# Performance work log

Measured on AMD Instinct MI355X. Metric: run time of the kernel, lower is better.

The kernel has to match this reference:

```python
import jax, jax.numpy as jnp
import numpy as np

N, E, IN, H, C = 20000, 320000, 512, 4, 64
HC = H * C
EPS_BN = 1e-5


def setup_inputs() -> dict:
    key = jax.random.key(0)
    ks = jax.random.split(key, 12)
    p = lambda k, shape, s=0.05: jax.random.normal(k, shape, dtype=jnp.float32) * s
    z = lambda n: jnp.zeros((n,), jnp.float32)
    o = lambda n: jnp.ones((n,), jnp.float32)
    return {
        "x": jax.random.normal(ks[0], (N, IN), dtype=jnp.float32),
        "edge_index": jax.random.randint(ks[1], (2, E), 0, N),
        "Wl0": p(ks[2], (IN, HC)), "Wr0": p(ks[3], (IN, HC)),
        "att0": p(ks[4], (H, C)), "b0": z(HC),
        "g0": o(HC), "be0": z(HC), "m0": z(HC), "v0": o(HC),
        "Wl1": p(ks[5], (HC, HC)), "Wr1": p(ks[6], (HC, HC)),
        "att1": p(ks[7], (H, C)), "b1": z(HC),
        "g1": o(HC), "be1": z(HC), "m1": z(HC), "v1": o(HC),
        "Wl2": p(ks[8], (HC, 2)), "Wr2": p(ks[9], (HC, 2)),
        "att2": p(ks[10], (1, 2)), "b2": z(2),
    }


def gatv2_conv(x, Wl, Wr, att, b, ei, concat):
    # GATv2: e_ij = att . LeakyReLU(Wl x_j + Wr x_i); softmax over in-edges of i
    n = x.shape[0]
    h, c = att.shape
    xl = (x @ Wl).reshape(n, h, c)  # source/message transform
    xr = (x @ Wr).reshape(n, h, c)  # target transform
    src, dst = ei[0], ei[1]
    m = xl[src] + xr[dst]                                   # [E,H,C] edge gather
    e = jnp.sum(jax.nn.leaky_relu(m, 0.2) * att, axis=-1)   # [E,H]
    emax = jax.ops.segment_max(e, dst, num_segments=n)      # segment softmax
    emax = jnp.where(jnp.isfinite(emax), emax, 0.0)
    ex = jnp.exp(e - emax[dst])
    denom = jax.ops.segment_sum(ex, dst, num_segments=n)
    alpha = ex / (denom[dst] + 1e-16)                       # [E,H]
    out = jax.ops.segment_sum(alpha[:, :, None] * xl[src], dst, num_segments=n)
    out = out.reshape(n, h * c) if concat else out.mean(axis=1)
    return out + b


def bn_eval(x, g, be, m, v):
    return (x - m) * (g * jax.lax.rsqrt(v + EPS_BN)) + be


def reference(x, edge_index, Wl0, Wr0, att0, b0, g0, be0, m0, v0,
              Wl1, Wr1, att1, b1, g1, be1, m1, v1, Wl2, Wr2, att2, b2):
    loops = jnp.arange(N)
    ei = jnp.concatenate([edge_index, jnp.stack([loops, loops])], axis=1)
    h = gatv2_conv(x, Wl0, Wr0, att0, b0, ei, True)
    h = jax.nn.elu(bn_eval(h, g0, be0, m0, v0))
    h = gatv2_conv(h, Wl1, Wr1, att1, b1, ei, True)
    h = jax.nn.elu(bn_eval(h, g1, be1, m1, v1))
    out = gatv2_conv(h, Wl2, Wr2, att2, b2, ei, False)
    return jax.nn.log_softmax(out, axis=1)
```

## Files before the change

kernel.cpp:

```cpp
#include <hip/hip_runtime.h>
#include <math.h>

#define NN 20000
#define MP 20096
#define EE 320000
#define ET (EE + NN)
#define HC 256
#define EPS_BN 1e-5f

typedef __bf16 bf16x8 __attribute__((ext_vector_type(8)));
typedef float f32x4 __attribute__((ext_vector_type(4)));

__device__ __forceinline__ float4 ld4(const float* p) { return *reinterpret_cast<const float4*>(p); }
__device__ __forceinline__ float lrelu(float x) { return fmaxf(x, 0.f) + 0.2f * fminf(x, 0.f); }

__device__ __forceinline__ unsigned short f2b(float f) {
  unsigned int u = __float_as_uint(f);
  u = (u + 0x7fffu + ((u >> 16) & 1u)) >> 16;
  return (unsigned short)u;
}
__device__ __forceinline__ float b2f(unsigned short u) {
  return __uint_as_float(((unsigned int)u) << 16);
}

__device__ __forceinline__ void gld_lds16(const void* g, void* l) {
  __builtin_amdgcn_global_load_lds(
      (const __attribute__((address_space(1))) unsigned int*)g,
      (__attribute__((address_space(3))) unsigned int*)(unsigned int)(unsigned long long)l,
      16, 0, 0);
}

#define CXB 5000
#define HB  ((ET + 255) / 256)
#define W0B 1024
#define W1B 512

__device__ __forceinline__ void conv_w_body(int idx, int K, const float* Wl, const float* Wr,
                                            unsigned short* Wf) {
  int n = idx / K, k = idx - n * K;
  float v = (n < 256) ? Wl[(size_t)k * 256 + n] : Wr[(size_t)k * 256 + (n - 256)];
  Wf[idx] = f2b(v);
}

__global__ __launch_bounds__(256) void prep_kernel(const float* __restrict__ x,
                                                   unsigned short* __restrict__ xb,
                                                   const int* __restrict__ ei,
                                                   int* __restrict__ counts,
                                                   const float* __restrict__ Wl0,
                                                   const float* __restrict__ Wr0,
                                                   unsigned short* __restrict__ Wf0,
                                                   const float* __restrict__ Wl1,
                                                   const float* __restrict__ Wr1,
                                                   unsigned short* __restrict__ Wf1) {
  const int b = blockIdx.x;
  if (b < CXB) {
    int i = (b * 256 + threadIdx.x) * 8;
    float4 v0 = ld4(&x[i]);
    float4 v1 = ld4(&x[i + 4]);
    ushort4 o0, o1;
    o0.x = f2b(v0.x); o0.y = f2b(v0.y); o0.z = f2b(v0.z); o0.w = f2b(v0.w);
    o1.x = f2b(v1.x); o1.y = f2b(v1.y); o1.z = f2b(v1.z); o1.w = f2b(v1.w);
    *reinterpret_cast<ushort4*>(&xb[i]) = o0;
    *reinterpret_cast<ushort4*>(&xb[i + 4]) = o1;
  } else if (b < CXB + HB) {
    int e = (b - CXB) * 256 + threadIdx.x;
    if (e < ET) {
      int d = (e < EE) ? ei[EE + e] : (e - EE);
      atomicAdd(&counts[d], 1);
    }
  } else if (b < CXB + HB + W0B) {
    conv_w_body((b - CXB - HB) * 256 + threadIdx.x, 512, Wl0, Wr0, Wf0);
  } else {
    conv_w_body((b - CXB - HB - W0B) * 256 + threadIdx.x, 256, Wl1, Wr1, Wf1);
  }
}

__global__ __launch_bounds__(512, 6) void gemm_mfma(const unsigned short* __restrict__ A,
                                                    const unsigned short* __restrict__ Bt,
                                                    unsigned short* __restrict__ xlb,
                                                    float* __restrict__ xrf,
                                                    int M, int K) {
  __shared__ unsigned short As[3][128 * 32];
  __shared__ unsigned short Bs[3][128 * 32];
  const int tid = threadIdx.x;
  const int wave = tid >> 6;
  const int lane = tid & 63;
  const int am = lane & 15;
  const int aq = lane >> 4;
  const int wr = (wave >> 2) * 64;
  const int wc = (wave & 3) * 32;

  const int nwg = gridDim.x;
  const int orig = blockIdx.x;
  const int q = nwg >> 3, r = nwg & 7;
  const int xcd = orig & 7, ii = orig >> 3;
  const int wgid = (xcd < r ? xcd * (q + 1) : r * (q + 1) + (xcd - r) * q) + ii;
  const int row0 = (wgid >> 2) * 128;
  const int col0 = (wgid & 3) * 128;

  const int r_ = tid >> 2;
  const int ks = (tid & 3) * 8;
  const size_t aoff = (size_t)(row0 + r_) * K + ks;
  const size_t boff = (size_t)(col0 + r_) * K + ks;

  const int nk = K >> 5;

#define STAGE(tt, bb)                                                    \
  do {                                                                   \
    gld_lds16(A + aoff + (size_t)(tt) * 32, &As[bb][wave * 512]);        \
    gld_lds16(Bt + boff + (size_t)(tt) * 32, &Bs[bb][wave * 512]);       \
  } while (0)

  f32x4 acc[4][2] = {};

  STAGE(0, 0);
  STAGE(1, 1);

  int cur = 0;
  int sb = 2;
  for (int t = 0; t < nk; ++t) {
    if (t + 1 < nk) {
      asm volatile("s_waitcnt vmcnt(2)" ::: "memory");
    } else {
      asm volatile("s_waitcnt vmcnt(0)" ::: "memory");
    }
    __builtin_amdgcn_s_barrier();
    __builtin_amdgcn_sched_barrier(0);

    if (t + 2 < nk) STAGE(t + 2, sb);

    bf16x8 af[4], bfr[2];
#pragma unroll
    for (int i = 0; i < 4; ++i)
      af[i] = *reinterpret_cast<const bf16x8*>(&As[cur][(wr + i * 16 + am) * 32 + aq * 8]);
#pragma unroll
    for (int j = 0; j < 2; ++j)
      bfr[j] = *reinterpret_cast<const bf16x8*>(&Bs[cur][(wc + j * 16 + am) * 32 + aq * 8]);
#pragma unroll
    for (int i = 0; i < 4; ++i)
#pragma unroll
      for (int j = 0; j < 2; ++j)
        acc[i][j] = __builtin_amdgcn_mfma_f32_16x16x32_bf16(af[i], bfr[j], acc[i][j], 0, 0, 0);

    cur = (cur == 2) ? 0 : cur + 1;
    sb = (sb == 2) ? 0 : sb + 1;
  }
#undef STAGE

#pragma unroll
  for (int i = 0; i < 4; ++i) {
#pragma unroll
    for (int j = 0; j < 2; ++j) {
      int gcol = col0 + wc + j * 16 + am;
#pragma unroll
      for (int rr = 0; rr < 4; ++rr) {
        int grow = row0 + wr + i * 16 + aq * 4 + rr;
        if (grow < M) {
          float v = acc[i][j][rr];
          if (gcol < 256) xlb[(size_t)grow * 256 + gcol] = f2b(v);
          else            xrf[(size_t)grow * 256 + (gcol - 256)] = v;
        }
      }
    }
  }
}

__global__ __launch_bounds__(1024) void scan_kernel(int* __restrict__ cursor,
                                                    int* __restrict__ offsets) {
  __shared__ int wsum[16];
  const int tid = threadIdx.x;
  const int lane = tid & 63, wv = tid >> 6;
  const int base = tid * 20;
  int vals[20];
  int s = 0;
  if (tid < 1000) {
#pragma unroll
    for (int j = 0; j < 20; ++j) { vals[j] = cursor[base + j]; s += vals[j]; }
  }
  int ssum = s;
#pragma unroll
  for (int off = 1; off < 64; off <<= 1) {
    int t = __shfl_up(ssum, off);
    if (lane >= off) ssum += t;
  }
  if (lane == 63) wsum[wv] = ssum;
  __syncthreads();
  if (wv == 0) {
    int w = (lane < 16) ? wsum[lane] : 0;
#pragma unroll
    for (int off = 1; off < 16; off <<= 1) {
      int t = __shfl_up(w, off);
      if (lane >= off) w += t;
    }
    if (lane < 16) wsum[lane] = w;
  }
  __syncthreads();
  int excl = ssum - s + (wv > 0 ? wsum[wv - 1] : 0);
  if (tid < 1000) {
    int run = excl;
#pragma unroll
    for (int j = 0; j < 20; ++j) { offsets[base + j] = run; cursor[base + j] = run; run += vals[j]; }
  }
  if (tid == 1023) offsets[NN] = wsum[15];
}

__global__ __launch_bounds__(256) void scatter_kernel(const int* __restrict__ ei,
                                                      int* __restrict__ cursor,
                                                      int* __restrict__ srcs) {
  int e = blockIdx.x * blockDim.x + threadIdx.x;
  if (e >= ET) return;
  int s, d;
  if (e < EE) { s = ei[e]; d = ei[EE + e]; } else { s = d = e - EE; }
  int pos = atomicAdd(&cursor[d], 1);
  srcs[pos] = s;
}

__global__ __launch_bounds__(256) void gat_layer(const unsigned short* __restrict__ xlb,
                                                 const float* __restrict__ xrf,
                                                 const float* __restrict__ att,
                                                 const float* __restrict__ bias,
                                                 const float* __restrict__ gam,
                                                 const float* __restrict__ bet,
                                                 const float* __restrict__ mean,
                                                 const float* __restrict__ var,
                                                 const int* __restrict__ offsets,
                                                 const int* __restrict__ srcs,
                                                 unsigned short* __restrict__ hb) {
  const int wave = threadIdx.x >> 6;
  const int lane = threadIdx.x & 63;
  const int node = blockIdx.x * 4 + wave;
  if (node >= NN) return;

  const float4 xr4 = ld4(&xrf[(size_t)node * HC + lane * 4]);
  const float4 a4 = ld4(&att[lane * 4]);
  const int beg = offsets[node];
  const int end = offsets[node + 1];

  float lA = 0.f, lB = 0.f;
  float4 OA = make_float4(0.f, 0.f, 0.f, 0.f);
  float4 OB = make_float4(0.f, 0.f, 0.f, 0.f);

  int i = beg;
  for (; i + 3 < end; i += 4) {
    int s0 = srcs[i], s1 = srcs[i + 1], s2 = srcs[i + 2], s3 = srcs[i + 3];
    ushort4 u0 = *reinterpret_cast<const ushort4*>(&xlb[(size_t)s0 * HC + lane * 4]);
    ushort4 u1 = *reinterpret_cast<const ushort4*>(&xlb[(size_t)s1 * HC + lane * 4]);
    ushort4 u2 = *reinterpret_cast<const ushort4*>(&xlb[(size_t)s2 * HC + lane * 4]);
    ushort4 u3 = *reinterpret_cast<const ushort4*>(&xlb[(size_t)s3 * HC + lane * 4]);
    float4 x0 = make_float4(b2f(u0.x), b2f(u0.y), b2f(u0.z), b2f(u0.w));
    float4 x1 = make_float4(b2f(u1.x), b2f(u1.y), b2f(u1.z), b2f(u1.w));
    float4 x2 = make_float4(b2f(u2.x), b2f(u2.y), b2f(u2.z), b2f(u2.w));
    float4 x3 = make_float4(b2f(u3.x), b2f(u3.y), b2f(u3.z), b2f(u3.w));
    float e0 = lrelu(x0.x + xr4.x) * a4.x + lrelu(x0.y + xr4.y) * a4.y +
               lrelu(x0.z + xr4.z) * a4.z + lrelu(x0.w + xr4.w) * a4.w;
    float e1 = lrelu(x1.x + xr4.x) * a4.x + lrelu(x1.y + xr4.y) * a4.y +
               lrelu(x1.z + xr4.z) * a4.z + lrelu(x1.w + xr4.w) * a4.w;
    float e2 = lrelu(x2.x + xr4.x) * a4.x + lrelu(x2.y + xr4.y) * a4.y +
               lrelu(x2.z + xr4.z) * a4.z + lrelu(x2.w + xr4.w) * a4.w;
    float e3 = lrelu(x3.x + xr4.x) * a4.x + lrelu(x3.y + xr4.y) * a4.y +
               lrelu(x3.z + xr4.z) * a4.z + lrelu(x3.w + xr4.w) * a4.w;
#pragma unroll
    for (int off = 1; off < 16; off <<= 1) {
      e0 += __shfl_xor(e0, off);
      e1 += __shfl_xor(e1, off);
      e2 += __shfl_xor(e2, off);
      e3 += __shfl_xor(e3, off);
    }
    float p0 = __expf(e0), p1 = __expf(e1), p2 = __expf(e2), p3 = __expf(e3);
    lA += p0; lB += p1; lA += p2; lB += p3;
    OA.x += p0 * x0.x; OA.y += p0 * x0.y; OA.z += p0 * x0.z; OA.w += p0 * x0.w;
    OB.x += p1 * x1.x; OB.y += p1 * x1.y; OB.z += p1 * x1.z; OB.w += p1 * x1.w;
    OA.x += p2 * x2.x; OA.y += p2 * x2.y; OA.z += p2 * x2.z; OA.w += p2 * x2.w;
    OB.x += p3 * x3.x; OB.y += p3 * x3.y; OB.z += p3 * x3.z; OB.w += p3 * x3.w;
  }
  for (; i < end; ++i) {
    int s = srcs[i];
    ushort4 u = *reinterpret_cast<const ushort4*>(&xlb[(size_t)s * HC + lane * 4]);
    float4 x0 = make_float4(b2f(u.x), b2f(u.y), b2f(u.z), b2f(u.w));
    float e = lrelu(x0.x + xr4.x) * a4.x + lrelu(x0.y + xr4.y) * a4.y +
              lrelu(x0.z + xr4.z) * a4.z + lrelu(x0.w + xr4.w) * a4.w;
#pragma unroll
    for (int off = 1; off < 16; off <<= 1) e += __shfl_xor(e, off);
    float p = __expf(e);
    lA += p;
    OA.x += p * x0.x; OA.y += p * x0.y; OA.z += p * x0.z; OA.w += p * x0.w;
  }
  float inv = 1.f / (lA + lB);
  float4 O = make_float4(OA.x + OB.x, OA.y + OB.y, OA.z + OB.z, OA.w + OB.w);

  float4 b4 = ld4(&bias[lane * 4]);
  float4 g4 = ld4(&gam[lane * 4]);
  float4 e4 = ld4(&bet[lane * 4]);
  float4 m4 = ld4(&mean[lane * 4]);
  float4 v4 = ld4(&var[lane * 4]);
  float y0 = O.x * inv + b4.x, y1 = O.y * inv + b4.y;
  float y2 = O.z * inv + b4.z, y3 = O.w * inv + b4.w;
  float z0 = (y0 - m4.x) * (g4.x * rsqrtf(v4.x + EPS_BN)) + e4.x;
  float z1 = (y1 - m4.y) * (g4.y * rsqrtf(v4.y + EPS_BN)) + e4.y;
  float z2 = (y2 - m4.z) * (g4.z * rsqrtf(v4.z + EPS_BN)) + e4.z;
  float z3 = (y3 - m4.w) * (g4.w * rsqrtf(v4.w + EPS_BN)) + e4.w;
  ushort4 r;
  r.x = f2b(z0 > 0.f ? z0 : expm1f(z0));
  r.y = f2b(z1 > 0.f ? z1 : expm1f(z1));
  r.z = f2b(z2 > 0.f ? z2 : expm1f(z2));
  r.w = f2b(z3 > 0.f ? z3 : expm1f(z3));
  *reinterpret_cast<ushort4*>(&hb[(size_t)node * HC + lane * 4]) = r;
}

__global__ __launch_bounds__(256) void lin2_kernel(const unsigned short* __restrict__ hb,
                                                   const float* __restrict__ Wl,
                                                   const float* __restrict__ Wr,
                                                   float* __restrict__ xl2,
                                                   float* __restrict__ xr2) {
  const int wave = threadIdx.x >> 6;
  const int lane = threadIdx.x & 63;
  const int node = blockIdx.x * 4 + wave;
  if (node >= NN) return;
  ushort4 h4 = *reinterpret_cast<const ushort4*>(&hb[(size_t)node * HC + lane * 4]);
  float hv[4] = {b2f(h4.x), b2f(h4.y), b2f(h4.z), b2f(h4.w)};
  float l0 = 0.f, l1 = 0.f, r0 = 0.f, r1 = 0.f;
#pragma unroll
  for (int j = 0; j < 4; ++j) {
    int row = lane * 4 + j;
    l0 += hv[j] * Wl[row * 2 + 0];
    l1 += hv[j] * Wl[row * 2 + 1];
    r0 += hv[j] * Wr[row * 2 + 0];
    r1 += hv[j] * Wr[row * 2 + 1];
  }
#pragma unroll
  for (int off = 1; off < 64; off <<= 1) {
    l0 += __shfl_xor(l0, off);
    l1 += __shfl_xor(l1, off);
    r0 += __shfl_xor(r0, off);
    r1 += __shfl_xor(r1, off);
  }
  if (lane == 0) {
    xl2[node * 2 + 0] = l0; xl2[node * 2 + 1] = l1;
    xr2[node * 2 + 0] = r0; xr2[node * 2 + 1] = r1;
  }
}

__global__ __launch_bounds__(256) void gat2_out_kernel(const float* __restrict__ xl2,
                                                       const float* __restrict__ xr2,
                                                       const float* __restrict__ att2,
                                                       const float* __restrict__ b2,
                                                       const int* __restrict__ offsets,
                                                       const int* __restrict__ srcs,
                                                       float* __restrict__ out) {
  const int wave = threadIdx.x >> 6;
  const int lane = threadIdx.x & 63;
  const int node = blockIdx.x * 4 + wave;
  if (node >= NN) return;
  const float a0 = att2[0], a1 = att2[1];
  const float xr0 = xr2[node * 2 + 0], xr1 = xr2[node * 2 + 1];
  const int beg = offsets[node], end = offsets[node + 1];

  float l = 0.f, o0 = 0.f, o1 = 0.f;
  for (int i = beg + lane; i < end; i += 64) {
    int s = srcs[i];
    float x0 = xl2[s * 2 + 0], x1 = xl2[s * 2 + 1];
    float e = lrelu(x0 + xr0) * a0 + lrelu(x1 + xr1) * a1;
    float p = __expf(e);
    l += p;
    o0 += p * x0;
    o1 += p * x1;
  }
#pragma unroll
  for (int off = 1; off < 64; off <<= 1) {
    l += __shfl_xor(l, off);
    o0 += __shfl_xor(o0, off);
    o1 += __shfl_xor(o1, off);
  }
  if (lane == 0) {
    float inv = 1.f / l;
    float t0 = o0 * inv + b2[0];
    float t1 = o1 * inv + b2[1];
    float mx = fmaxf(t0, t1);
    float ls = mx + logf(__expf(t0 - mx) + __expf(t1 - mx));
    out[node * 2 + 0] = t0 - ls;
    out[node * 2 + 1] = t1 - ls;
  }
}

extern "C" void kernel_launch(void* const* d_in, const int* in_sizes, int n_in,
                              void* d_out, int out_size, void* d_ws, size_t ws_size,
                              hipStream_t stream) {
  const float* x    = (const float*)d_in[0];
  const int*   ei   = (const int*)d_in[1];
  const float* Wl0  = (const float*)d_in[2];
  const float* Wr0  = (const float*)d_in[3];
  const float* att0 = (const float*)d_in[4];
  const float* b0   = (const float*)d_in[5];
  const float* g0   = (const float*)d_in[6];
  const float* be0  = (const float*)d_in[7];
  const float* m0   = (const float*)d_in[8];
  const float* v0   = (const float*)d_in[9];
  const float* Wl1  = (const float*)d_in[10];
  const float* Wr1  = (const float*)d_in[11];
  const float* att1 = (const float*)d_in[12];
  const float* b1   = (const float*)d_in[13];
  const float* g1   = (const float*)d_in[14];
  const float* be1  = (const float*)d_in[15];
  const float* m1   = (const float*)d_in[16];
  const float* v1   = (const float*)d_in[17];
  const float* Wl2  = (const float*)d_in[18];
  const float* Wr2  = (const float*)d_in[19];
  const float* att2 = (const float*)d_in[20];
  const float* b2   = (const float*)d_in[21];

  float* xrf = (float*)d_ws;
  unsigned short* xlb = (unsigned short*)(xrf + (size_t)NN * 256);
  unsigned short* hb  = xlb + (size_t)NN * 256;
  unsigned short* xb  = hb + (size_t)MP * 256;
  unsigned short* Wf0 = xb + (size_t)MP * 512;
  unsigned short* Wf1 = Wf0 + 512 * 512;
  float* xl2 = (float*)(Wf1 + 512 * 256);
  float* xr2 = xl2 + 2 * NN;
  int* offsets = (int*)(xr2 + 2 * NN);
  int* cursor  = offsets + (NN + 1);
  int* srcs    = cursor + NN;

  hipMemsetAsync(cursor, 0, NN * sizeof(int), stream);
  prep_kernel<<<CXB + HB + W0B + W1B, 256, 0, stream>>>(x, xb, ei, cursor,
                                                        Wl0, Wr0, Wf0, Wl1, Wr1, Wf1);
  scan_kernel<<<1, 1024, 0, stream>>>(cursor, offsets);
  scatter_kernel<<<(ET + 255) / 256, 256, 0, stream>>>(ei, cursor, srcs);

  const int gemm_blocks = (MP / 128) * 4;
  gemm_mfma<<<gemm_blocks, 512, 0, stream>>>(xb, Wf0, xlb, xrf, NN, 512);
  gat_layer<<<NN / 4, 256, 0, stream>>>(xlb, xrf, att0, b0, g0, be0, m0, v0, offsets, srcs, hb);
  gemm_mfma<<<gemm_blocks, 512, 0, stream>>>(hb, Wf1, xlb, xrf, NN, 256);
  gat_layer<<<NN / 4, 256, 0, stream>>>(xlb, xrf, att1, b1, g1, be1, m1, v1, offsets, srcs, hb);
  lin2_kernel<<<NN / 4, 256, 0, stream>>>(hb, Wl2, Wr2, xl2, xr2);
  gat2_out_kernel<<<NN / 4, 256, 0, stream>>>(xl2, xr2, att2, b2, offsets, srcs, (float*)d_out);
}
```

Before: 286.5 us.

## Fuse degree histogram into single-block scan and fold lin2 into GAT layer

The per-destination degree counting moves out of the grid-wide prep kernel into a single 1024-thread block that builds the histogram with LDS atomics and then scans it, removing a memset and global atomics. The final linear projection to two outputs is fused into the second GAT layer epilogue, skipping the bf16 hidden-state write and a separate kernel. The trade-off is that one block must stream all edges serially, which may lengthen the critical path.

Result: slower. 360.9 us (+26.0%).

```diff
diff --git a/kernel.cpp b/kernel.cpp
--- a/kernel.cpp
+++ b/kernel.cpp
@@ -31,7 +31,6 @@
 }
 
 #define CXB 5000
-#define HB  ((ET + 255) / 256)
 #define W0B 1024
 #define W1B 512
 
@@ -44,8 +43,6 @@
 
 __global__ __launch_bounds__(256) void prep_kernel(const float* __restrict__ x,
                                                    unsigned short* __restrict__ xb,
-                                                   const int* __restrict__ ei,
-                                                   int* __restrict__ counts,
                                                    const float* __restrict__ Wl0,
                                                    const float* __restrict__ Wr0,
                                                    unsigned short* __restrict__ Wf0,
@@ -62,17 +59,72 @@
     o1.x = f2b(v1.x); o1.y = f2b(v1.y); o1.z = f2b(v1.z); o1.w = f2b(v1.w);
     *reinterpret_cast<ushort4*>(&xb[i]) = o0;
     *reinterpret_cast<ushort4*>(&xb[i + 4]) = o1;
-  } else if (b < CXB + HB) {
-    int e = (b - CXB) * 256 + threadIdx.x;
-    if (e < ET) {
-      int d = (e < EE) ? ei[EE + e] : (e - EE);
-      atomicAdd(&counts[d], 1);
-    }
-  } else if (b < CXB + HB + W0B) {
-    conv_w_body((b - CXB - HB) * 256 + threadIdx.x, 512, Wl0, Wr0, Wf0);
+  } else if (b < CXB + W0B) {
+    conv_w_body((b - CXB) * 256 + threadIdx.x, 512, Wl0, Wr0, Wf0);
   } else {
-    conv_w_body((b - CXB - HB - W0B) * 256 + threadIdx.x, 256, Wl1, Wr1, Wf1);
-  }
+    conv_w_body((b - CXB - W0B) * 256 + threadIdx.x, 256, Wl1, Wr1, Wf1);
+  }
+}
+
+__global__ __launch_bounds__(1024) void csr_scan_kernel(const int* __restrict__ ei,
+                                                        int* __restrict__ cursor,
+                                                        int* __restrict__ offsets) {
+  __shared__ int cnt[NN];
+  __shared__ int wsum[16];
+  const int tid = threadIdx.x;
+  const int lane = tid & 63, wv = tid >> 6;
+
+  for (int j = tid; j < NN; j += 1024) cnt[j] = 0;
+  __syncthreads();
+  for (int e = tid; e < ET; e += 1024) {
+    int d = (e < EE) ? ei[EE + e] : (e - EE);
+    atomicAdd(&cnt[d], 1);
+  }
+  __syncthreads();
+
+  const int base = tid * 20;
+  int vals[20];
+  int s = 0;
+  if (tid < 1000) {
+#pragma unroll
+    for (int j = 0; j < 20; ++j) { vals[j] = cnt[base + j]; s += vals[j]; }
+  }
+  int ssum = s;
+#pragma unroll
+  for (int off = 1; off < 64; off <<= 1) {
+    int t = __shfl_up(ssum, off);
+    if (lane >= off) ssum += t;
+  }
+  if (lane == 63) wsum[wv] = ssum;
+  __syncthreads();
+  if (wv == 0) {
+    int w = (lane < 16) ? wsum[lane] : 0;
+#pragma unroll
+    for (int off = 1; off < 16; off <<= 1) {
+      int t = __shfl_up(w, off);
+      if (lane >= off) w += t;
+    }
+    if (lane < 16) wsum[lane] = w;
+  }
+  __syncthreads();
+  int excl = ssum - s + (wv > 0 ? wsum[wv - 1] : 0);
+  if (tid < 1000) {
+    int run = excl;
+#pragma unroll
+    for (int j = 0; j < 20; ++j) { offsets[base + j] = run; cursor[base + j] = run; run += vals[j]; }
+  }
+  if (tid == 1023) offsets[NN] = wsum[15];
+}
+
+__global__ __launch_bounds__(256) void scatter_kernel(const int* __restrict__ ei,
+                                                      int* __restrict__ cursor,
+                                                      int* __restrict__ srcs) {
+  int e = blockIdx.x * blockDim.x + threadIdx.x;
+  if (e >= ET) return;
+  int s, d;
+  if (e < EE) { s = ei[e]; d = ei[EE + e]; } else { s = d = e - EE; }
+  int pos = atomicAdd(&cursor[d], 1);
+  srcs[pos] = s;
 }
 
 __global__ __launch_bounds__(512, 6) void gemm_mfma(const unsigned short* __restrict__ A,
@@ -165,56 +217,6 @@
   }
 }
 
-__global__ __launch_bounds__(1024) void scan_kernel(int* __restrict__ cursor,
-                                                    int* __restrict__ offsets) {
-  __shared__ int wsum[16];
-  const int tid = threadIdx.x;
-  const int lane = tid & 63, wv = tid >> 6;
-  const int base = tid * 20;
-  int vals[20];
-  int s = 0;
-  if (tid < 1000) {
-#pragma unroll
-    for (int j = 0; j < 20; ++j) { vals[j] = cursor[base + j]; s += vals[j]; }
-  }
-  int ssum = s;
-#pragma unroll
-  for (int off = 1; off < 64; off <<= 1) {
-    int t = __shfl_up(ssum, off);
-    if (lane >= off) ssum += t;
-  }
-  if (lane == 63) wsum[wv] = ssum;
-  __syncthreads();
-  if (wv == 0) {
-    int w = (lane < 16) ? wsum[lane] : 0;
-#pragma unroll
-    for (int off = 1; off < 16; off <<= 1) {
-      int t = __shfl_up(w, off);
-      if (lane >= off) w += t;
-    }
-    if (lane < 16) wsum[lane] = w;
-  }
-  __syncthreads();
-  int excl = ssum - s + (wv > 0 ? wsum[wv - 1] : 0);
-  if (tid < 1000) {
-    int run = excl;
-#pragma unroll
-    for (int j = 0; j < 20; ++j) { offsets[base + j] = run; cursor[base + j] = run; run += vals[j]; }
-  }
-  if (tid == 1023) offsets[NN] = wsum[15];
-}
-
-__global__ __launch_bounds__(256) void scatter_kernel(const int* __restrict__ ei,
-                                                      int* __restrict__ cursor,
-                                                      int* __restrict__ srcs) {
-  int e = blockIdx.x * blockDim.x + threadIdx.x;
-  if (e >= ET) return;
-  int s, d;
-  if (e < EE) { s = ei[e]; d = ei[EE + e]; } else { s = d = e - EE; }
-  int pos = atomicAdd(&cursor[d], 1);
-  srcs[pos] = s;
-}
-
 __global__ __launch_bounds__(256) void gat_layer(const unsigned short* __restrict__ xlb,
                                                  const float* __restrict__ xrf,
                                                  const float* __restrict__ att,
@@ -225,7 +227,11 @@
                                                  const float* __restrict__ var,
                                                  const int* __restrict__ offsets,
                                                  const int* __restrict__ srcs,
-                                                 unsigned short* __restrict__ hb) {
+                                                 unsigned short* __restrict__ hb,
+                                                 const float* __restrict__ Wl2,
+                                                 const float* __restrict__ Wr2,
+                                                 float* __restrict__ xl2,
+                                                 float* __restrict__ xr2) {
   const int wave = threadIdx.x >> 6;
   const int lane = threadIdx.x & 63;
   const int node = blockIdx.x * 4 + wave;
@@ -299,44 +305,37 @@
   float z1 = (y1 - m4.y) * (g4.y * rsqrtf(v4.y + EPS_BN)) + e4.y;
   float z2 = (y2 - m4.z) * (g4.z * rsqrtf(v4.z + EPS_BN)) + e4.z;
   float z3 = (y3 - m4.w) * (g4.w * rsqrtf(v4.w + EPS_BN)) + e4.w;
-  ushort4 r;
-  r.x = f2b(z0 > 0.f ? z0 : expm1f(z0));
-  r.y = f2b(z1 > 0.f ? z1 : expm1f(z1));
-  r.z = f2b(z2 > 0.f ? z2 : expm1f(z2));
-  r.w = f2b(z3 > 0.f ? z3 : expm1f(z3));
-  *reinterpret_cast<ushort4*>(&hb[(size_t)node * HC + lane * 4]) = r;
-}
-
-__global__ __launch_bounds__(256) void lin2_kernel(const unsigned short* __restrict__ hb,
-                                                   const float* __restrict__ Wl,
-                                                   const float* __restrict__ Wr,
-                                                   float* __restrict__ xl2,
-                                                   float* __restrict__ xr2) {
-  const int wave = threadIdx.x >> 6;
-  const int lane = threadIdx.x & 63;
-  const int node = blockIdx.x * 4 + wave;
-  if (node >= NN) return;
-  ushort4 h4 = *reinterpret_cast<const ushort4*>(&hb[(size_t)node * HC + lane * 4]);
-  float hv[4] = {b2f(h4.x), b2f(h4.y), b2f(h4.z), b2f(h4.w)};
-  float l0 = 0.f, l1 = 0.f, r0 = 0.f, r1 = 0.f;
-#pragma unroll
-  for (int j = 0; j < 4; ++j) {
-    int row = lane * 4 + j;
-    l0 += hv[j] * Wl[row * 2 + 0];
-    l1 += hv[j] * Wl[row * 2 + 1];
-    r0 += hv[j] * Wr[row * 2 + 0];
-    r1 += hv[j] * Wr[row * 2 + 1];
-  }
-#pragma unroll
-  for (int off = 1; off < 64; off <<= 1) {
-    l0 += __shfl_xor(l0, off);
-    l1 += __shfl_xor(l1, off);
-    r0 += __shfl_xor(r0, off);
-    r1 += __shfl_xor(r1, off);
-  }
-  if (lane == 0) {
-    xl2[node * 2 + 0] = l0; xl2[node * 2 + 1] = l1;
-    xr2[node * 2 + 0] = r0; xr2[node * 2 + 1] = r1;
+  z0 = z0 > 0.f ? z0 : expm1f(z0);
+  z1 = z1 > 0.f ? z1 : expm1f(z1);
+  z2 = z2 > 0.f ? z2 : expm1f(z2);
+  z3 = z3 > 0.f ? z3 : expm1f(z3);
+
+  if (Wl2 != nullptr) {
+    float zz[4] = {z0, z1, z2, z3};
+    float l0 = 0.f, l1 = 0.f, r0 = 0.f, r1 = 0.f;
+#pragma unroll
+    for (int j = 0; j < 4; ++j) {
+      int row = lane * 4 + j;
+      l0 += zz[j] * Wl2[row * 2 + 0];
+      l1 += zz[j] * Wl2[row * 2 + 1];
+      r0 += zz[j] * Wr2[row * 2 + 0];
+      r1 += zz[j] * Wr2[row * 2 + 1];
+    }
+#pragma unroll
+    for (int off = 1; off < 64; off <<= 1) {
+      l0 += __shfl_xor(l0, off);
+      l1 += __shfl_xor(l1, off);
+      r0 += __shfl_xor(r0, off);
+      r1 += __shfl_xor(r1, off);
+    }
+    if (lane == 0) {
+      xl2[node * 2 + 0] = l0; xl2[node * 2 + 1] = l1;
+      xr2[node * 2 + 0] = r0; xr2[node * 2 + 1] = r1;
+    }
+  } else {
+    ushort4 r;
+    r.x = f2b(z0); r.y = f2b(z1); r.z = f2b(z2); r.w = f2b(z3);
+    *reinterpret_cast<ushort4*>(&hb[(size_t)node * HC + lane * 4]) = r;
   }
 }
 
@@ -420,17 +419,16 @@
   int* cursor  = offsets + (NN + 1);
   int* srcs    = cursor + NN;
 
-  hipMemsetAsync(cursor, 0, NN * sizeof(int), stream);
-  prep_kernel<<<CXB + HB + W0B + W1B, 256, 0, stream>>>(x, xb, ei, cursor,
-                                                        Wl0, Wr0, Wf0, Wl1, Wr1, Wf1);
-  scan_kernel<<<1, 1024, 0, stream>>>(cursor, offsets);
+  prep_kernel<<<CXB + W0B + W1B, 256, 0, stream>>>(x, xb, Wl0, Wr0, Wf0, Wl1, Wr1, Wf1);
+  csr_scan_kernel<<<1, 1024, 0, stream>>>(ei, cursor, offsets);
   scatter_kernel<<<(ET + 255) / 256, 256, 0, stream>>>(ei, cursor, srcs);
 
   const int gemm_blocks = (MP / 128) * 4;
   gemm_mfma<<<gemm_blocks, 512, 0, stream>>>(xb, Wf0, xlb, xrf, NN, 512);
-  gat_layer<<<NN / 4, 256, 0, stream>>>(xlb, xrf, att0, b0, g0, be0, m0, v0, offsets, srcs, hb);
+  gat_layer<<<NN / 4, 256, 0, stream>>>(xlb, xrf, att0, b0, g0, be0, m0, v0, offsets, srcs, hb,
+                                        nullptr, nullptr, nullptr, nullptr);
   gemm_mfma<<<gemm_blocks, 512, 0, stream>>>(hb, Wf1, xlb, xrf, NN, 256);
-  gat_layer<<<NN / 4, 256, 0, stream>>>(xlb, xrf, att1, b1, g1, be1, m1, v1, offsets, srcs, hb);
-  lin2_kernel<<<NN / 4, 256, 0, stream>>>(hb, Wl2, Wr2, xl2, xr2);
+  gat_layer<<<NN / 4, 256, 0, stream>>>(xlb, xrf, att1, b1, g1, be1, m1, v1, offsets, srcs, hb,
+                                        Wl2, Wr2, xl2, xr2);
   gat2_out_kernel<<<NN / 4, 256, 0, stream>>>(xl2, xr2, att2, b2, offsets, srcs, (float*)d_out);
 }
```
